# Kernel optimization log

Measured on AMD Instinct MI355X. Metric: run time of the kernel, lower is better.

Reference implementation:

```python
import jax, jax.numpy as jnp
import numpy as np

N_NODES = 100000
N_EDGES = 1600000
DIM = 64
LAYERS = 2


def setup_inputs() -> dict:
    key = jax.random.key(0)
    k1, k2, k3, k4 = jax.random.split(key, 4)
    h = jax.random.normal(k1, (N_NODES, DIM), dtype=jnp.float32)
    w = jax.random.uniform(k2, (N_EDGES,), dtype=jnp.float32)
    src = jax.random.randint(k3, (N_EDGES,), 0, N_NODES, dtype=jnp.int32)
    dst = jax.random.randint(k4, (N_EDGES,), 0, N_NODES, dtype=jnp.int32)
    return {"h": h, "w": w, "src": src, "dst": dst}


def reference(h, w, src, dst):
    N = h.shape[0]
    # weighted in-degree, clamped at 1 (DGL in_degrees(weight='w').clamp(min=1))
    deg = jnp.maximum(jax.ops.segment_sum(w, dst, num_segments=N), 1.0)
    norm = deg[:, None] ** -0.5  # [N, 1]
    embs = [h]
    for _ in range(LAYERS):
        h_norm = h * norm                              # [N, d]
        m = h_norm[src] * w[:, None]                   # [E, d] edge messages (u_mul_e)
        neigh_sum = jax.ops.segment_sum(m, dst, num_segments=N)  # fn.sum
        h = neigh_sum * norm
        embs.append(h)
    # mean over [h0, h1, ..., hL]
    return jnp.mean(jnp.stack(embs, axis=1), axis=1)
```

## Files before the change

kernel.cpp:

```cpp
#include <hip/hip_runtime.h>
#include <hip/hip_bf16.h>

#define D 64
#define THREADS 256
#define BKT_BITS 9
#define BKT_NODES (1 << BKT_BITS)
#define CHUNK 4096

__device__ __forceinline__ unsigned f2bf(float f) {
    unsigned u = __float_as_uint(f);
    return (u + 0x7fffu + ((u >> 16) & 1u)) >> 16;
}
__device__ __forceinline__ float2 bfpair(unsigned v) {
    return make_float2(__uint_as_float(v << 16), __uint_as_float(v & 0xffff0000u));
}

typedef float f32x4 __attribute__((ext_vector_type(4)));
typedef unsigned u32x4 __attribute__((ext_vector_type(4)));
__device__ __forceinline__ void stnt_f4(float4 v, float4* p) {
    f32x4 t = {v.x, v.y, v.z, v.w};
    __builtin_nontemporal_store(t, (f32x4*)p);
}
__device__ __forceinline__ void stnt_u4(uint4 v, uint4* p) {
    u32x4 t = {v.x, v.y, v.z, v.w};
    __builtin_nontemporal_store(t, (u32x4*)p);
}

__global__ void p1a_hist(const int* __restrict__ dst, int* __restrict__ blockCount,
                         const float* __restrict__ h, unsigned* __restrict__ hbf2,
                         long long nd4, int E, int B) {
    __shared__ int lc[256];
    int t = threadIdx.x;
    lc[t] = 0;
    __syncthreads();
    for (long long i = (long long)blockIdx.x * THREADS + t; i < nd4;
         i += (long long)gridDim.x * THREADS) {
        float4 v = ((const float4*)h)[i];
        ((uint2*)hbf2)[i] = make_uint2(f2bf(v.x) | (f2bf(v.y) << 16),
                                       f2bf(v.z) | (f2bf(v.w) << 16));
    }
    int base = blockIdx.x * CHUNK;
    int end = min(base + CHUNK, E);
    int end4 = end >> 2;
    for (int e4 = (base >> 2) + t; e4 < end4; e4 += THREADS) {
        int4 d4 = ((const int4*)dst)[e4];
        atomicAdd(&lc[d4.x >> BKT_BITS], 1);
        atomicAdd(&lc[d4.y >> BKT_BITS], 1);
        atomicAdd(&lc[d4.z >> BKT_BITS], 1);
        atomicAdd(&lc[d4.w >> BKT_BITS], 1);
    }
    for (int e = (end4 << 2) + t; e < end; e += THREADS)
        atomicAdd(&lc[dst[e] >> BKT_BITS], 1);
    __syncthreads();
    if (t < B) blockCount[(long long)blockIdx.x * B + t] = lc[t];
}

__global__ void p1b_scanblocks(int* __restrict__ blockCount, int* __restrict__ total,
                               int NBLK, int B) {
    __shared__ int sm[256];
    int b = blockIdx.x, t = threadIdx.x;
    int run = 0;
    for (int base = 0; base < NBLK; base += 256) {
        int i = base + t;
        int v = (i < NBLK) ? blockCount[(long long)i * B + b] : 0;
        sm[t] = v;
        __syncthreads();
        for (int off = 1; off < 256; off <<= 1) {
            int u = (t >= off) ? sm[t - off] : 0;
            __syncthreads();
            sm[t] += u;
            __syncthreads();
        }
        if (i < NBLK) blockCount[(long long)i * B + b] = run + sm[t] - v;
        run += sm[255];
        __syncthreads();
    }
    if (t == 0) total[b] = run;
}

__global__ void p1c_scanbuckets(const int* __restrict__ total, int* __restrict__ bstart,
                                int B, int E) {
    __shared__ int sm[256];
    int t = threadIdx.x;
    int run = 0;
    for (int base = 0; base < B; base += 256) {
        int i = base + t;
        int v = (i < B) ? total[i] : 0;
        sm[t] = v;
        __syncthreads();
        for (int off = 1; off < 256; off <<= 1) {
            int u = (t >= off) ? sm[t - off] : 0;
            __syncthreads();
            sm[t] += u;
            __syncthreads();
        }
        if (i < B) bstart[i] = run + sm[t] - v;
        run += sm[255];
        __syncthreads();
    }
    if (t == 0) bstart[B] = E;
}

__global__ void p1d_scatter(const int* __restrict__ dst, const int* __restrict__ src,
                            const float* __restrict__ w, const int* __restrict__ blockCount,
                            const int* __restrict__ bstart, int2* __restrict__ temp,
                            int E, int B) {
    __shared__ int cur[256];
    int t = threadIdx.x;
    if (t < B) cur[t] = bstart[t] + blockCount[(long long)blockIdx.x * B + t];
    __syncthreads();
    int base = blockIdx.x * CHUNK;
    int end = min(base + CHUNK, E);
    int end4 = end >> 2;
    for (int e4 = (base >> 2) + t; e4 < end4; e4 += THREADS) {
        int4 d4 = ((const int4*)dst)[e4];
        int4 s4 = ((const int4*)src)[e4];
        float4 w4 = ((const float4*)w)[e4];
        int pos;
        pos = atomicAdd(&cur[d4.x >> BKT_BITS], 1);
        temp[pos] = make_int2(s4.x | ((d4.x & (BKT_NODES - 1)) << 17), __float_as_int(w4.x));
        pos = atomicAdd(&cur[d4.y >> BKT_BITS], 1);
        temp[pos] = make_int2(s4.y | ((d4.y & (BKT_NODES - 1)) << 17), __float_as_int(w4.y));
        pos = atomicAdd(&cur[d4.z >> BKT_BITS], 1);
        temp[pos] = make_int2(s4.z | ((d4.z & (BKT_NODES - 1)) << 17), __float_as_int(w4.z));
        pos = atomicAdd(&cur[d4.w >> BKT_BITS], 1);
        temp[pos] = make_int2(s4.w | ((d4.w & (BKT_NODES - 1)) << 17), __float_as_int(w4.w));
    }
    for (int e = (end4 << 2) + t; e < end; e += THREADS) {
        int d = dst[e];
        int pos = atomicAdd(&cur[d >> BKT_BITS], 1);
        temp[pos] = make_int2(src[e] | ((d & (BKT_NODES - 1)) << 17), __float_as_int(w[e]));
    }
}

__global__ void p2_build(const int2* __restrict__ temp, const int* __restrict__ bstart,
                         int2* __restrict__ packed, int* __restrict__ rowptr,
                         float* __restrict__ norm, int N, int E, int B) {
    __shared__ int cnt[BKT_NODES];
    __shared__ float degs[BKT_NODES];
    __shared__ int cur[BKT_NODES];
    __shared__ int sm[256];
    int b = blockIdx.x, t = threadIdx.x;
    int ebeg = bstart[b], eend = bstart[b + 1];
    for (int i = t; i < BKT_NODES; i += THREADS) { cnt[i] = 0; degs[i] = 0.0f; }
    __syncthreads();
    for (int e = ebeg + t; e < eend; e += THREADS) {
        int2 pk = temp[e];
        int dl = (pk.x >> 17) & (BKT_NODES - 1);
        atomicAdd(&cnt[dl], 1);
        atomicAdd(&degs[dl], __int_as_float(pk.y));
    }
    __syncthreads();
    int run = 0;
    for (int base = 0; base < BKT_NODES; base += 256) {
        int v = cnt[base + t];
        sm[t] = v;
        __syncthreads();
        for (int off = 1; off < 256; off <<= 1) {
            int u = (t >= off) ? sm[t - off] : 0;
            __syncthreads();
            sm[t] += u;
            __syncthreads();
        }
        cur[base + t] = run + sm[t] - v;
        run += sm[255];
        __syncthreads();
    }
    int node0 = b << BKT_BITS;
    for (int i = t; i < BKT_NODES; i += THREADS) {
        int node = node0 + i;
        if (node < N) {
            rowptr[node] = ebeg + cur[i];
            norm[node] = rsqrtf(fmaxf(degs[i], 1.0f));
        }
    }
    if (b == 0 && t == 0) rowptr[N] = E;
    __syncthreads();
    for (int e = ebeg + t; e < eend; e += THREADS) {
        int2 pk = temp[e];
        int dl = (pk.x >> 17) & (BKT_NODES - 1);
        int pos = atomicAdd(&cur[dl], 1);
        packed[ebeg + pos] = make_int2(pk.x & 0x1ffff, pk.y);
    }
}

#define EDGE_FMA(r, c, A0, A1, A2, A3, A4, A5, A6, A7) do {            \
    float2 fa = bfpair((r).x), fb = bfpair((r).y);                      \
    float2 fc = bfpair((r).z), fd = bfpair((r).w);                      \
    A0 = fmaf(fa.x, (c), A0); A1 = fmaf(fa.y, (c), A1);                 \
    A2 = fmaf(fb.x, (c), A2); A3 = fmaf(fb.y, (c), A3);                 \
    A4 = fmaf(fc.x, (c), A4); A5 = fmaf(fc.y, (c), A5);                 \
    A6 = fmaf(fd.x, (c), A6); A7 = fmaf(fd.y, (c), A7); } while (0)

__global__ void gather1_kernel(const uint4* __restrict__ h_in, const int2* __restrict__ packed,
                               const int* __restrict__ rowptr, const float* __restrict__ norm,
                               uint4* __restrict__ h_out, int N) {
    int node = blockIdx.x * (blockDim.x >> 3) + (threadIdx.x >> 3);
    int lane = threadIdx.x & 7;
    if (node >= N) return;
    int j = rowptr[node], end = rowptr[node + 1];
    float a0 = 0, a1 = 0, a2 = 0, a3 = 0, a4 = 0, a5 = 0, a6 = 0, a7 = 0;
    float b0 = 0, b1 = 0, b2 = 0, b3 = 0, b4 = 0, b5 = 0, b6 = 0, b7 = 0;
    for (; j + 8 <= end; j += 8) {
        int2 p0 = packed[j + 0], p1 = packed[j + 1], p2 = packed[j + 2], p3 = packed[j + 3];
        int2 p4 = packed[j + 4], p5 = packed[j + 5], p6 = packed[j + 6], p7 = packed[j + 7];
        uint4 r0 = h_in[((long long)p0.x << 3) + lane];
        uint4 r1 = h_in[((long long)p1.x << 3) + lane];
        uint4 r2 = h_in[((long long)p2.x << 3) + lane];
        uint4 r3 = h_in[((long long)p3.x << 3) + lane];
        uint4 r4 = h_in[((long long)p4.x << 3) + lane];
        uint4 r5 = h_in[((long long)p5.x << 3) + lane];
        uint4 r6 = h_in[((long long)p6.x << 3) + lane];
        uint4 r7 = h_in[((long long)p7.x << 3) + lane];
        float c0 = __int_as_float(p0.y) * norm[p0.x];
        float c1 = __int_as_float(p1.y) * norm[p1.x];
        float c2 = __int_as_float(p2.y) * norm[p2.x];
        float c3 = __int_as_float(p3.y) * norm[p3.x];
        float c4 = __int_as_float(p4.y) * norm[p4.x];
        float c5 = __int_as_float(p5.y) * norm[p5.x];
        float c6 = __int_as_float(p6.y) * norm[p6.x];
        float c7 = __int_as_float(p7.y) * norm[p7.x];
        EDGE_FMA(r0, c0, a0, a1, a2, a3, a4, a5, a6, a7);
        EDGE_FMA(r1, c1, b0, b1, b2, b3, b4, b5, b6, b7);
        EDGE_FMA(r2, c2, a0, a1, a2, a3, a4, a5, a6, a7);
        EDGE_FMA(r3, c3, b0, b1, b2, b3, b4, b5, b6, b7);
        EDGE_FMA(r4, c4, a0, a1, a2, a3, a4, a5, a6, a7);
        EDGE_FMA(r5, c5, b0, b1, b2, b3, b4, b5, b6, b7);
        EDGE_FMA(r6, c6, a0, a1, a2, a3, a4, a5, a6, a7);
        EDGE_FMA(r7, c7, b0, b1, b2, b3, b4, b5, b6, b7);
    }
    for (; j + 4 <= end; j += 4) {
        int2 p0 = packed[j + 0], p1 = packed[j + 1], p2 = packed[j + 2], p3 = packed[j + 3];
        uint4 r0 = h_in[((long long)p0.x << 3) + lane];
        uint4 r1 = h_in[((long long)p1.x << 3) + lane];
        uint4 r2 = h_in[((long long)p2.x << 3) + lane];
        uint4 r3 = h_in[((long long)p3.x << 3) + lane];
        float c0 = __int_as_float(p0.y) * norm[p0.x];
        float c1 = __int_as_float(p1.y) * norm[p1.x];
        float c2 = __int_as_float(p2.y) * norm[p2.x];
        float c3 = __int_as_float(p3.y) * norm[p3.x];
        EDGE_FMA(r0, c0, a0, a1, a2, a3, a4, a5, a6, a7);
        EDGE_FMA(r1, c1, b0, b1, b2, b3, b4, b5, b6, b7);
        EDGE_FMA(r2, c2, a0, a1, a2, a3, a4, a5, a6, a7);
        EDGE_FMA(r3, c3, b0, b1, b2, b3, b4, b5, b6, b7);
    }
    for (; j < end; ++j) {
        int2 p = packed[j];
        uint4 r = h_in[((long long)p.x << 3) + lane];
        float c = __int_as_float(p.y) * norm[p.x];
        EDGE_FMA(r, c, a0, a1, a2, a3, a4, a5, a6, a7);
    }
    float nv = norm[node];
    float d0 = (a0 + b0) * nv, d1 = (a1 + b1) * nv, d2 = (a2 + b2) * nv, d3 = (a3 + b3) * nv;
    float d4 = (a4 + b4) * nv, d5 = (a5 + b5) * nv, d6 = (a6 + b6) * nv, d7 = (a7 + b7) * nv;
    stnt_u4(make_uint4(f2bf(d0) | (f2bf(d1) << 16), f2bf(d2) | (f2bf(d3) << 16),
                       f2bf(d4) | (f2bf(d5) << 16), f2bf(d6) | (f2bf(d7) << 16)),
            &h_out[((long long)node << 3) + lane]);
}

__global__ void gather2_final_kernel(const uint4* __restrict__ h0bf, const uint4* __restrict__ h1bf,
                                     const int2* __restrict__ packed, const int* __restrict__ rowptr,
                                     const float* __restrict__ norm, float* __restrict__ out, int N) {
    int node = blockIdx.x * (blockDim.x >> 3) + (threadIdx.x >> 3);
    int lane = threadIdx.x & 7;
    if (node >= N) return;
    int j = rowptr[node], end = rowptr[node + 1];
    float a0 = 0, a1 = 0, a2 = 0, a3 = 0, a4 = 0, a5 = 0, a6 = 0, a7 = 0;
    float b0 = 0, b1 = 0, b2 = 0, b3 = 0, b4 = 0, b5 = 0, b6 = 0, b7 = 0;
    for (; j + 8 <= end; j += 8) {
        int2 p0 = packed[j + 0], p1 = packed[j + 1], p2 = packed[j + 2], p3 = packed[j + 3];
        int2 p4 = packed[j + 4], p5 = packed[j + 5], p6 = packed[j + 6], p7 = packed[j + 7];
        uint4 r0 = h1bf[((long long)p0.x << 3) + lane];
        uint4 r1 = h1bf[((long long)p1.x << 3) + lane];
        uint4 r2 = h1bf[((long long)p2.x << 3) + lane];
        uint4 r3 = h1bf[((long long)p3.x << 3) + lane];
        uint4 r4 = h1bf[((long long)p4.x << 3) + lane];
        uint4 r5 = h1bf[((long long)p5.x << 3) + lane];
        uint4 r6 = h1bf[((long long)p6.x << 3) + lane];
        uint4 r7 = h1bf[((long long)p7.x << 3) + lane];
        float c0 = __int_as_float(p0.y) * norm[p0.x];
        float c1 = __int_as_float(p1.y) * norm[p1.x];
        float c2 = __int_as_float(p2.y) * norm[p2.x];
        float c3 = __int_as_float(p3.y) * norm[p3.x];
        float c4 = __int_as_float(p4.y) * norm[p4.x];
        float c5 = __int_as_float(p5.y) * norm[p5.x];
        float c6 = __int_as_float(p6.y) * norm[p6.x];
        float c7 = __int_as_float(p7.y) * norm[p7.x];
        EDGE_FMA(r0, c0, a0, a1, a2, a3, a4, a5, a6, a7);
        EDGE_FMA(r1, c1, b0, b1, b2, b3, b4, b5, b6, b7);
        EDGE_FMA(r2, c2, a0, a1, a2, a3, a4, a5, a6, a7);
        EDGE_FMA(r3, c3, b0, b1, b2, b3, b4, b5, b6, b7);
        EDGE_FMA(r4, c4, a0, a1, a2, a3, a4, a5, a6, a7);
        EDGE_FMA(r5, c5, b0, b1, b2, b3, b4, b5, b6, b7);
        EDGE_FMA(r6, c6, a0, a1, a2, a3, a4, a5, a6, a7);
        EDGE_FMA(r7, c7, b0, b1, b2, b3, b4, b5, b6, b7);
    }
    for (; j + 4 <= end; j += 4) {
        int2 p0 = packed[j + 0], p1 = packed[j + 1], p2 = packed[j + 2], p3 = packed[j + 3];
        uint4 r0 = h1bf[((long long)p0.x << 3) + lane];
        uint4 r1 = h1bf[((long long)p1.x << 3) + lane];
        uint4 r2 = h1bf[((long long)p2.x << 3) + lane];
        uint4 r3 = h1bf[((long long)p3.x << 3) + lane];
        float c0 = __int_as_float(p0.y) * norm[p0.x];
        float c1 = __int_as_float(p1.y) * norm[p1.x];
        float c2 = __int_as_float(p2.y) * norm[p2.x];
        float c3 = __int_as_float(p3.y) * norm[p3.x];
        EDGE_FMA(r0, c0, a0, a1, a2, a3, a4, a5, a6, a7);
        EDGE_FMA(r1, c1, b0, b1, b2, b3, b4, b5, b6, b7);
        EDGE_FMA(r2, c2, a0, a1, a2, a3, a4, a5, a6, a7);
        EDGE_FMA(r3, c3, b0, b1, b2, b3, b4, b5, b6, b7);
    }
    for (; j < end; ++j) {
        int2 p = packed[j];
        uint4 r = h1bf[((long long)p.x << 3) + lane];
        float c = __int_as_float(p.y) * norm[p.x];
        EDGE_FMA(r, c, a0, a1, a2, a3, a4, a5, a6, a7);
    }
    long long idx = ((long long)node << 3) + lane;
    float nv = norm[node];
    uint4 h0r = h0bf[idx];
    uint4 h1r = h1bf[idx];
    float2 h0a = bfpair(h0r.x), h0b = bfpair(h0r.y), h0c = bfpair(h0r.z), h0d = bfpair(h0r.w);
    float2 h1a = bfpair(h1r.x), h1b = bfpair(h1r.y), h1c = bfpair(h1r.z), h1d = bfpair(h1r.w);
    float4 o0, o1;
    o0.x = (h0a.x + h1a.x + (a0 + b0) * nv) * (1.0f / 3.0f);
    o0.y = (h0a.y + h1a.y + (a1 + b1) * nv) * (1.0f / 3.0f);
    o0.z = (h0b.x + h1b.x + (a2 + b2) * nv) * (1.0f / 3.0f);
    o0.w = (h0b.y + h1b.y + (a3 + b3) * nv) * (1.0f / 3.0f);
    o1.x = (h0c.x + h1c.x + (a4 + b4) * nv) * (1.0f / 3.0f);
    o1.y = (h0c.y + h1c.y + (a5 + b5) * nv) * (1.0f / 3.0f);
    o1.z = (h0d.x + h1d.x + (a6 + b6) * nv) * (1.0f / 3.0f);
    o1.w = (h0d.y + h1d.y + (a7 + b7) * nv) * (1.0f / 3.0f);
    stnt_f4(o0, &((float4*)out)[((long long)node << 4) + (lane << 1)]);
    stnt_f4(o1, &((float4*)out)[((long long)node << 4) + (lane << 1) + 1]);
}

extern "C" void kernel_launch(void* const* d_in, const int* in_sizes, int n_in,
                              void* d_out, int out_size, void* d_ws, size_t ws_size,
                              hipStream_t stream) {
    const float* h   = (const float*)d_in[0];
    const float* w   = (const float*)d_in[1];
    const int*   src = (const int*)d_in[2];
    const int*   dst = (const int*)d_in[3];
    const int N = in_sizes[0] / D;
    const int E = in_sizes[1];
    float* out = (float*)d_out;

    const int B = (N + BKT_NODES - 1) >> BKT_BITS;
    const int NBLK = (E + CHUNK - 1) / CHUNK;

    char* ws = (char*)d_ws;
    size_t off = 0;
    auto alloc = [&](size_t bytes, size_t align) -> char* {
        off = (off + align - 1) & ~(align - 1);
        char* p = ws + off;
        off += bytes;
        return p;
    };
    float* norm     = (float*)alloc((size_t)N * 4, 16);
    int*   rowptr   = (int*)  alloc((size_t)(N + 1) * 4, 16);
    int*   total    = (int*)  alloc((size_t)B * 4, 16);
    int*   bstart   = (int*)  alloc((size_t)(B + 1) * 4, 16);
    int*   blockCnt = (int*)  alloc((size_t)NBLK * B * 4, 16);
    int2*  packed   = (int2*) alloc((size_t)E * 8, 128);
    char*  shared_region = alloc((size_t)E * 8, 128);
    int2*     temp = (int2*)shared_region;
    unsigned* h1bf = (unsigned*)shared_region;
    unsigned* h0bf = (unsigned*)alloc((size_t)N * D * 2, 128);

    const int nodes_per_block = THREADS / 8;
    const int gather_blocks = (N + nodes_per_block - 1) / nodes_per_block;
    const long long nd4 = (long long)N * D / 4;

    p1a_hist<<<NBLK, THREADS, 0, stream>>>(dst, blockCnt, h, h0bf, nd4, E, B);
    p1b_scanblocks<<<B, 256, 0, stream>>>(blockCnt, total, NBLK, B);
    p1c_scanbuckets<<<1, 256, 0, stream>>>(total, bstart, B, E);
    p1d_scatter<<<NBLK, THREADS, 0, stream>>>(dst, src, w, blockCnt, bstart, temp, E, B);
    p2_build<<<B, 256, 0, stream>>>(temp, bstart, packed, rowptr, norm, N, E, B);

    gather1_kernel<<<gather_blocks, THREADS, 0, stream>>>((const uint4*)h0bf, packed, rowptr,
                                                          norm, (uint4*)h1bf, N);
    gather2_final_kernel<<<gather_blocks, THREADS, 0, stream>>>((const uint4*)h0bf, (const uint4*)h1bf,
                                                                packed, rowptr, norm, out, N);
}
```

Before: 220.0 us.

## Sort nodes by in-degree within buckets to balance gather wavefront work

The CSR build now counting-sorts the nodes of each 512-node bucket by edge count and writes a per-slot (start, node|count) descriptor in place of rowptr. The two gather kernels walk these descriptors, so each wavefront processes nodes of similar degree and loop-trip divergence across its node groups is reduced. In exchange there is an extra shared-memory sort in p2_build, less locality in output writes, and node ids and counts are packed into 17 bits each, which limits N and per-node degree.

```diff
diff --git a/kernel.cpp b/kernel.cpp
--- a/kernel.cpp
+++ b/kernel.cpp
@@ -134,15 +134,18 @@
 }
 
 __global__ void p2_build(const int2* __restrict__ temp, const int* __restrict__ bstart,
-                         int2* __restrict__ packed, int* __restrict__ rowptr,
+                         int2* __restrict__ packed, int2* __restrict__ vinfo,
                          float* __restrict__ norm, int N, int E, int B) {
     __shared__ int cnt[BKT_NODES];
     __shared__ float degs[BKT_NODES];
     __shared__ int cur[BKT_NODES];
     __shared__ int sm[256];
+    __shared__ int dbin[64];
+    __shared__ int perm[BKT_NODES];
     int b = blockIdx.x, t = threadIdx.x;
     int ebeg = bstart[b], eend = bstart[b + 1];
     for (int i = t; i < BKT_NODES; i += THREADS) { cnt[i] = 0; degs[i] = 0.0f; }
+    if (t < 64) dbin[t] = 0;
     __syncthreads();
     for (int e = ebeg + t; e < eend; e += THREADS) {
         int2 pk = temp[e];
@@ -169,12 +172,24 @@
     int node0 = b << BKT_BITS;
     for (int i = t; i < BKT_NODES; i += THREADS) {
         int node = node0 + i;
-        if (node < N) {
-            rowptr[node] = ebeg + cur[i];
-            norm[node] = rsqrtf(fmaxf(degs[i], 1.0f));
-        }
-    }
-    if (b == 0 && t == 0) rowptr[N] = E;
+        if (node < N) norm[node] = rsqrtf(fmaxf(degs[i], 1.0f));
+        atomicAdd(&dbin[min(cnt[i], 63)], 1);
+    }
+    __syncthreads();
+    if (t == 0) {
+        int r = 0;
+        for (int k = 0; k < 64; ++k) { int v = dbin[k]; dbin[k] = r; r += v; }
+    }
+    __syncthreads();
+    for (int i = t; i < BKT_NODES; i += THREADS) {
+        int pos = atomicAdd(&dbin[min(cnt[i], 63)], 1);
+        perm[pos] = i;
+    }
+    __syncthreads();
+    for (int v = t; v < BKT_NODES; v += THREADS) {
+        int i = perm[v];
+        vinfo[node0 + v] = make_int2(ebeg + cur[i], (node0 + i) | (cnt[i] << 17));
+    }
     __syncthreads();
     for (int e = ebeg + t; e < eend; e += THREADS) {
         int2 pk = temp[e];
@@ -193,12 +208,13 @@
     A6 = fmaf(fd.x, (c), A6); A7 = fmaf(fd.y, (c), A7); } while (0)
 
 __global__ void gather1_kernel(const uint4* __restrict__ h_in, const int2* __restrict__ packed,
-                               const int* __restrict__ rowptr, const float* __restrict__ norm,
+                               const int2* __restrict__ vinfo, const float* __restrict__ norm,
                                uint4* __restrict__ h_out, int N) {
-    int node = blockIdx.x * (blockDim.x >> 3) + (threadIdx.x >> 3);
+    int v = blockIdx.x * (blockDim.x >> 3) + (threadIdx.x >> 3);
     int lane = threadIdx.x & 7;
-    if (node >= N) return;
-    int j = rowptr[node], end = rowptr[node + 1];
+    int2 vi = vinfo[v];
+    int node = vi.y & 0x1ffff;
+    int j = vi.x, end = j + (vi.y >> 17);
     float a0 = 0, a1 = 0, a2 = 0, a3 = 0, a4 = 0, a5 = 0, a6 = 0, a7 = 0;
     float b0 = 0, b1 = 0, b2 = 0, b3 = 0, b4 = 0, b5 = 0, b6 = 0, b7 = 0;
     for (; j + 8 <= end; j += 8) {
@@ -250,21 +266,24 @@
         float c = __int_as_float(p.y) * norm[p.x];
         EDGE_FMA(r, c, a0, a1, a2, a3, a4, a5, a6, a7);
     }
-    float nv = norm[node];
-    float d0 = (a0 + b0) * nv, d1 = (a1 + b1) * nv, d2 = (a2 + b2) * nv, d3 = (a3 + b3) * nv;
-    float d4 = (a4 + b4) * nv, d5 = (a5 + b5) * nv, d6 = (a6 + b6) * nv, d7 = (a7 + b7) * nv;
-    stnt_u4(make_uint4(f2bf(d0) | (f2bf(d1) << 16), f2bf(d2) | (f2bf(d3) << 16),
-                       f2bf(d4) | (f2bf(d5) << 16), f2bf(d6) | (f2bf(d7) << 16)),
-            &h_out[((long long)node << 3) + lane]);
+    if (node < N) {
+        float nv = norm[node];
+        float d0 = (a0 + b0) * nv, d1 = (a1 + b1) * nv, d2 = (a2 + b2) * nv, d3 = (a3 + b3) * nv;
+        float d4 = (a4 + b4) * nv, d5 = (a5 + b5) * nv, d6 = (a6 + b6) * nv, d7 = (a7 + b7) * nv;
+        stnt_u4(make_uint4(f2bf(d0) | (f2bf(d1) << 16), f2bf(d2) | (f2bf(d3) << 16),
+                           f2bf(d4) | (f2bf(d5) << 16), f2bf(d6) | (f2bf(d7) << 16)),
+                &h_out[((long long)node << 3) + lane]);
+    }
 }
 
 __global__ void gather2_final_kernel(const uint4* __restrict__ h0bf, const uint4* __restrict__ h1bf,
-                                     const int2* __restrict__ packed, const int* __restrict__ rowptr,
+                                     const int2* __restrict__ packed, const int2* __restrict__ vinfo,
                                      const float* __restrict__ norm, float* __restrict__ out, int N) {
-    int node = blockIdx.x * (blockDim.x >> 3) + (threadIdx.x >> 3);
+    int v = blockIdx.x * (blockDim.x >> 3) + (threadIdx.x >> 3);
     int lane = threadIdx.x & 7;
-    if (node >= N) return;
-    int j = rowptr[node], end = rowptr[node + 1];
+    int2 vi = vinfo[v];
+    int node = vi.y & 0x1ffff;
+    int j = vi.x, end = j + (vi.y >> 17);
     float a0 = 0, a1 = 0, a2 = 0, a3 = 0, a4 = 0, a5 = 0, a6 = 0, a7 = 0;
     float b0 = 0, b1 = 0, b2 = 0, b3 = 0, b4 = 0, b5 = 0, b6 = 0, b7 = 0;
     for (; j + 8 <= end; j += 8) {
@@ -316,23 +335,25 @@
         float c = __int_as_float(p.y) * norm[p.x];
         EDGE_FMA(r, c, a0, a1, a2, a3, a4, a5, a6, a7);
     }
-    long long idx = ((long long)node << 3) + lane;
-    float nv = norm[node];
-    uint4 h0r = h0bf[idx];
-    uint4 h1r = h1bf[idx];
-    float2 h0a = bfpair(h0r.x), h0b = bfpair(h0r.y), h0c = bfpair(h0r.z), h0d = bfpair(h0r.w);
-    float2 h1a = bfpair(h1r.x), h1b = bfpair(h1r.y), h1c = bfpair(h1r.z), h1d = bfpair(h1r.w);
-    float4 o0, o1;
-    o0.x = (h0a.x + h1a.x + (a0 + b0) * nv) * (1.0f / 3.0f);
-    o0.y = (h0a.y + h1a.y + (a1 + b1) * nv) * (1.0f / 3.0f);
-    o0.z = (h0b.x + h1b.x + (a2 + b2) * nv) * (1.0f / 3.0f);
-    o0.w = (h0b.y + h1b.y + (a3 + b3) * nv) * (1.0f / 3.0f);
-    o1.x = (h0c.x + h1c.x + (a4 + b4) * nv) * (1.0f / 3.0f);
-    o1.y = (h0c.y + h1c.y + (a5 + b5) * nv) * (1.0f / 3.0f);
-    o1.z = (h0d.x + h1d.x + (a6 + b6) * nv) * (1.0f / 3.0f);
-    o1.w = (h0d.y + h1d.y + (a7 + b7) * nv) * (1.0f / 3.0f);
-    stnt_f4(o0, &((float4*)out)[((long long)node << 4) + (lane << 1)]);
-    stnt_f4(o1, &((float4*)out)[((long long)node << 4) + (lane << 1) + 1]);
+    if (node < N) {
+        long long idx = ((long long)node << 3) + lane;
+        float nv = norm[node];
+        uint4 h0r = h0bf[idx];
+        uint4 h1r = h1bf[idx];
+        float2 h0a = bfpair(h0r.x), h0b = bfpair(h0r.y), h0c = bfpair(h0r.z), h0d = bfpair(h0r.w);
+        float2 h1a = bfpair(h1r.x), h1b = bfpair(h1r.y), h1c = bfpair(h1r.z), h1d = bfpair(h1r.w);
+        float4 o0, o1;
+        o0.x = (h0a.x + h1a.x + (a0 + b0) * nv) * (1.0f / 3.0f);
+        o0.y = (h0a.y + h1a.y + (a1 + b1) * nv) * (1.0f / 3.0f);
+        o0.z = (h0b.x + h1b.x + (a2 + b2) * nv) * (1.0f / 3.0f);
+        o0.w = (h0b.y + h1b.y + (a3 + b3) * nv) * (1.0f / 3.0f);
+        o1.x = (h0c.x + h1c.x + (a4 + b4) * nv) * (1.0f / 3.0f);
+        o1.y = (h0c.y + h1c.y + (a5 + b5) * nv) * (1.0f / 3.0f);
+        o1.z = (h0d.x + h1d.x + (a6 + b6) * nv) * (1.0f / 3.0f);
+        o1.w = (h0d.y + h1d.y + (a7 + b7) * nv) * (1.0f / 3.0f);
+        stnt_f4(o0, &((float4*)out)[((long long)node << 4) + (lane << 1)]);
+        stnt_f4(o1, &((float4*)out)[((long long)node << 4) + (lane << 1) + 1]);
+    }
 }
 
 extern "C" void kernel_launch(void* const* d_in, const int* in_sizes, int n_in,
@@ -347,6 +368,7 @@
     float* out = (float*)d_out;
 
     const int B = (N + BKT_NODES - 1) >> BKT_BITS;
+    const int NPAD = B << BKT_BITS;
     const int NBLK = (E + CHUNK - 1) / CHUNK;
 
     char* ws = (char*)d_ws;
@@ -358,10 +380,10 @@
         return p;
     };
     float* norm     = (float*)alloc((size_t)N * 4, 16);
-    int*   rowptr   = (int*)  alloc((size_t)(N + 1) * 4, 16);
     int*   total    = (int*)  alloc((size_t)B * 4, 16);
     int*   bstart   = (int*)  alloc((size_t)(B + 1) * 4, 16);
     int*   blockCnt = (int*)  alloc((size_t)NBLK * B * 4, 16);
+    int2*  vinfo    = (int2*) alloc((size_t)NPAD * 8, 16);
     int2*  packed   = (int2*) alloc((size_t)E * 8, 128);
     char*  shared_region = alloc((size_t)E * 8, 128);
     int2*     temp = (int2*)shared_region;
@@ -369,17 +391,17 @@
     unsigned* h0bf = (unsigned*)alloc((size_t)N * D * 2, 128);
 
     const int nodes_per_block = THREADS / 8;
-    const int gather_blocks = (N + nodes_per_block - 1) / nodes_per_block;
+    const int gather_blocks = NPAD / nodes_per_block;
     const long long nd4 = (long long)N * D / 4;
 
     p1a_hist<<<NBLK, THREADS, 0, stream>>>(dst, blockCnt, h, h0bf, nd4, E, B);
     p1b_scanblocks<<<B, 256, 0, stream>>>(blockCnt, total, NBLK, B);
     p1c_scanbuckets<<<1, 256, 0, stream>>>(total, bstart, B, E);
     p1d_scatter<<<NBLK, THREADS, 0, stream>>>(dst, src, w, blockCnt, bstart, temp, E, B);
-    p2_build<<<B, 256, 0, stream>>>(temp, bstart, packed, rowptr, norm, N, E, B);
-
-    gather1_kernel<<<gather_blocks, THREADS, 0, stream>>>((const uint4*)h0bf, packed, rowptr,
+    p2_build<<<B, 256, 0, stream>>>(temp, bstart, packed, vinfo, norm, N, E, B);
+
+    gather1_kernel<<<gather_blocks, THREADS, 0, stream>>>((const uint4*)h0bf, packed, vinfo,
                                                           norm, (uint4*)h1bf, N);
     gather2_final_kernel<<<gather_blocks, THREADS, 0, stream>>>((const uint4*)h0bf, (const uint4*)h1bf,
-                                                                packed, rowptr, norm, out, N);
-}
+                                                                packed, vinfo, norm, out, N);
+}
```

Measured after the change: 235.9 us. +7.2%, slower.
